# Optimization experiments

Measured on AMD Instinct MI355X. Metric: run time of the kernel, lower is better.

Reference implementation:

```python
import jax, jax.numpy as jnp
import numpy as np

B, S, E = 2, 2048, 1024
HID = 1024
HEADS = 16
EPS = 1e-5
SCALE = (E * 2) ** (-0.5)  # source uses input_data_dim*2


def setup_inputs() -> dict:
    key = jax.random.key(0)
    k1, k2, k3 = jax.random.split(key, 3)
    return {
        "x": jax.random.normal(k1, (B, S, E), dtype=jnp.float32),
        "ln_g": jnp.ones((E,), jnp.float32),
        "ln_b": jnp.zeros((E,), jnp.float32),
        "W1": jax.random.normal(k2, (E, 3 * HID), jnp.float32) * 0.02,
        "b1": jnp.zeros((3 * HID,), jnp.float32),
        "W2": jax.random.normal(k3, (HID, HID), jnp.float32) * 0.02,
        "b2": jnp.zeros((HID,), jnp.float32),
    }


def reference(x, ln_g, ln_b, W1, b1, W2, b2):
    # LayerNorm over last dim
    mu = jnp.mean(x, axis=-1, keepdims=True)
    var = jnp.mean(jnp.square(x - mu), axis=-1, keepdims=True)
    xn = (x - mu) * jax.lax.rsqrt(var + EPS) * ln_g + ln_b
    # QKV projection: [B,S,3*HID]
    qkv = jnp.einsum('bse,ef->bsf', xn, W1) + b1
    # Faithful to source: flat reshape to (heads, B, S, 3*HID/heads)
    qkv_heads = qkv.reshape(HEADS, B, S, -1)
    q, k, v = jnp.split(qkv_heads, 3, axis=-1)  # each [H,B,S,d]
    scores = jnp.einsum('hbse,hbSe->hbsS', q, k) * SCALE  # [H,B,S,S]
    att = jax.nn.softmax(scores, axis=-1)
    full_att = jnp.einsum('hbsS,hbSe->hbse', att, v)  # [H,B,S,d]
    full_att = full_att.reshape(B, S, -1)  # faithful flat reshape -> [B,S,HID]
    out = jnp.einsum('bsh,hk->bsk', full_att, W2) + b2
    return out
```

## Files before the change

kernel.cpp:

```cpp
#include <hip/hip_runtime.h>

typedef unsigned short u16;
typedef __bf16 bf16x8 __attribute__((ext_vector_type(8)));
typedef float f32x4 __attribute__((ext_vector_type(4)));

static constexpr float SCALE2 = 0.022097086912079608f * 1.4426950408889634f;

__device__ __forceinline__ u16 f2b(float f) {
  union { float f; unsigned int i; } v; v.f = f;
  unsigned int r = v.i + 0x7fffu + ((v.i >> 16) & 1u);
  return (u16)(r >> 16);
}
__device__ __forceinline__ unsigned int pk2(float a, float b) {
#if __has_builtin(__builtin_amdgcn_cvt_pk_bf16_f32)
  auto v = __builtin_amdgcn_cvt_pk_bf16_f32(a, b);
  unsigned int u;
  __builtin_memcpy(&u, &v, 4);
  return u;
#else
  union { float f; unsigned int i; } x, y; x.f = a; y.f = b;
  return ((x.i + 0x8000u) >> 16) | ((y.i + 0x8000u) & 0xffff0000u);
#endif
}
__device__ __forceinline__ void async16(const u16* g, u16* l) {
  __builtin_amdgcn_global_load_lds((const __attribute__((address_space(1))) void*)g,
                                   (__attribute__((address_space(3))) void*)l,
                                   16, 0, 0);
}

__global__ __launch_bounds__(256) void pre_kernel(const float* __restrict__ x,
                                                  const float* __restrict__ lg,
                                                  const float* __restrict__ lb,
                                                  u16* __restrict__ xn,
                                                  const float* __restrict__ W1,
                                                  u16* __restrict__ W1T,
                                                  const float* __restrict__ W2,
                                                  u16* __restrict__ W2T) {
  __shared__ __align__(16) u16 smem[64 * 72];
  const int bx = blockIdx.x;
  const int t = threadIdx.x;
  if (bx < 4096) {
    float* red = (float*)smem;
    const int row = bx;
    float4 v = *(const float4*)(x + (size_t)row * 1024 + t * 4);
    float s = v.x + v.y + v.z + v.w;
    float ss = v.x * v.x + v.y * v.y + v.z * v.z + v.w * v.w;
    for (int off = 32; off >= 1; off >>= 1) {
      s += __shfl_xor(s, off, 64);
      ss += __shfl_xor(ss, off, 64);
    }
    const int w = t >> 6;
    if ((t & 63) == 0) { red[w] = s; red[4 + w] = ss; }
    __syncthreads();
    s = red[0] + red[1] + red[2] + red[3];
    ss = red[4] + red[5] + red[6] + red[7];
    const float mu = s * (1.0f / 1024.0f);
    const float var = ss * (1.0f / 1024.0f) - mu * mu;
    const float inv = rsqrtf(var + 1e-5f);
    float4 gg = *(const float4*)(lg + t * 4);
    float4 bb = *(const float4*)(lb + t * 4);
    ushort4 o;
    o.x = f2b((v.x - mu) * inv * gg.x + bb.x);
    o.y = f2b((v.y - mu) * inv * gg.y + bb.y);
    o.z = f2b((v.z - mu) * inv * gg.z + bb.z);
    o.w = f2b((v.w - mu) * inv * gg.w + bb.w);
    *(ushort4*)(xn + (size_t)row * 1024 + t * 4) = o;
    return;
  }
  const float* in;
  u16* out;
  int C, c0, r0;
  if (bx < 4096 + 768) {
    const int idx = bx - 4096;
    C = 3072; in = W1; out = W1T;
    c0 = (idx % 48) * 64; r0 = (idx / 48) * 64;
  } else {
    const int idx = bx - 4864;
    C = 1024; in = W2; out = W2T;
    c0 = (idx % 16) * 64; r0 = (idx / 16) * 64;
  }
  const int row = t >> 2, cseg = t & 3;
  for (int it = 0; it < 4; it++) {
    float4 v = *(const float4*)&in[(size_t)(r0 + row) * C + c0 + it * 16 + cseg * 4];
    ushort4 o;
    o.x = f2b(v.x); o.y = f2b(v.y); o.z = f2b(v.z); o.w = f2b(v.w);
    *(ushort4*)&smem[row * 72 + it * 16 + cseg * 4] = o;
  }
  __syncthreads();
  const int orow = t >> 2, ch = t & 3;
  u16 vals[16];
  for (int j = 0; j < 16; j++) vals[j] = smem[(ch * 16 + j) * 72 + orow];
  u16* dp = out + (size_t)(c0 + orow) * 1024 + r0 + ch * 16;
  *(uint4*)&dp[0] = *(uint4*)&vals[0];
  *(uint4*)&dp[8] = *(uint4*)&vals[8];
}

template <int MODE, int MT>
__global__ __launch_bounds__(256) void gemm_bt(const u16* __restrict__ A,
                                               const u16* __restrict__ Bt,
                                               const float* __restrict__ bias,
                                               float* __restrict__ C,
                                               int M, int N, int K,
                                               u16* __restrict__ Qc,
                                               u16* __restrict__ Kc,
                                               u16* __restrict__ Vtmp) {
  __shared__ __align__(16) u16 SMEM[8192];
  u16* As = SMEM;
  u16* Bs = SMEM + MT * 32;
  const int m0 = blockIdx.y * MT, n0 = blockIdx.x * 128;
  const int t = threadIdx.x, w = t >> 6, lane = t & 63;
  const int q = lane >> 4, l16 = lane & 15;
  const int wm = (w >> 1) * (MT / 2), wn = (w & 1) * 64;
  constexpr int NI = MT / 32;

  const int sc = (lane & 3) ^ ((lane >> 3) & 3);
  const u16* ap = A + (size_t)(m0 + w * 16 + (lane >> 2)) * K + sc * 8;
  const u16* bp = Bt + (size_t)(n0 + w * 16 + (lane >> 2)) * K + sc * 8;
  u16* lA = &As[w * 512];
  u16* lB = &Bs[w * 512];
  const int ac = q ^ ((l16 >> 1) & 3);

  f32x4 acc[NI][4];
  const f32x4 zero = {0.f, 0.f, 0.f, 0.f};
  for (int i = 0; i < NI; i++)
    for (int j = 0; j < 4; j++) acc[i][j] = zero;

  for (int k0 = 0; k0 < K; k0 += 32) {
    for (int i = 0; i < MT / 64; i++)
      async16(ap + (size_t)(i * 64) * K, lA + i * 2048);
    for (int i = 0; i < 2; i++)
      async16(bp + (size_t)(i * 64) * K, lB + i * 2048);
    ap += 32; bp += 32;
    __syncthreads();
    bf16x8 af[NI], bfr[4];
    for (int i = 0; i < NI; i++)
      af[i] = *(const bf16x8*)&As[(wm + i * 16 + l16) * 32 + ac * 8];
    for (int j = 0; j < 4; j++)
      bfr[j] = *(const bf16x8*)&Bs[(wn + j * 16 + l16) * 32 + ac * 8];
    for (int i = 0; i < NI; i++)
      for (int j = 0; j < 4; j++)
        acc[i][j] = __builtin_amdgcn_mfma_f32_16x16x32_bf16(af[i], bfr[j], acc[i][j], 0, 0, 0);
    __syncthreads();
  }

  if constexpr (MODE == 0) {
    for (int j = 0; j < 4; j++) {
      const int col = n0 + wn + j * 16 + l16;
      const float bv = bias[col];
      for (int i = 0; i < NI; i++) {
        const int rbase = m0 + wm + i * 16 + q * 4;
        for (int r = 0; r < 4; r++)
          C[(size_t)(rbase + r) * N + col] = acc[i][j][r] + bv;
      }
    }
  } else {
    const int seg = n0 + wn;
    const int k64 = seg >> 6;
    const int tcol = k64 / 3;
    const int typ = k64 - tcol * 3;
    u16* dst = (typ == 0) ? Qc : (typ == 1) ? Kc : Vtmp;
    const float qs = (typ == 0) ? SCALE2 : 1.0f;
    const int gidx = m0 >> 7;
    u16* tw = &SMEM[w * 1280];
    float bv[4];
    for (int j = 0; j < 4; j++) bv[j] = bias[seg + j * 16 + l16];
    __syncthreads();
    for (int i = 0; i < 4; i++) {
      for (int j = 0; j < 4; j++) {
        ushort4 pk;
        pk.x = f2b((acc[i][j][0] + bv[j]) * qs);
        pk.y = f2b((acc[i][j][1] + bv[j]) * qs);
        pk.z = f2b((acc[i][j][2] + bv[j]) * qs);
        pk.w = f2b((acc[i][j][3] + bv[j]) * qs);
        *(ushort4*)&tw[(j * 16 + l16) * 20 + q * 4] = pk;
      }
      const int r2 = lane >> 2;
      const int quarter = lane & 3;
      u16 vals[16];
      for (int c = 0; c < 16; c++)
        vals[c] = tw[(quarter * 16 + c) * 20 + r2];
      const int lr = wm + i * 16 + r2;
      const int s = (lr << 4) + tcol;
      u16* dp = dst + ((size_t)gidx * 2048 + s) * 64 + quarter * 16;
      *(uint4*)&dp[0] = *(uint4*)&vals[0];
      *(uint4*)&dp[8] = *(uint4*)&vals[8];
    }
  }
}

__global__ __launch_bounds__(256) void vtrans(const u16* __restrict__ Vtmp,
                                              u16* __restrict__ Vt) {
  __shared__ __align__(16) u16 tile[64 * 64];
  const int g = blockIdx.y, s0 = blockIdx.x * 64;
  const int t = threadIdx.x;
  const int row = t >> 3, ch = t & 7;
  for (int p = 0; p < 2; p++) {
    const int r = p * 32 + row;
    uint4 v = *(const uint4*)&Vtmp[((size_t)g * 2048 + s0 + r) * 64 + ch * 8];
    *(uint4*)&tile[r * 64 + ((ch ^ (r & 7)) * 8)] = v;
  }
  __syncthreads();
  const int d = t >> 2, scn = t & 3;
  u16 vals[16];
  for (int j2 = 0; j2 < 16; j2++) {
    const int s = scn * 16 + j2;
    vals[j2] = tile[s * 64 + (((d >> 3) ^ (s & 7)) * 8) + (d & 7)];
  }
  u16* dp = Vt + ((size_t)g * 64 + d) * 2048 + s0 + scn * 16;
  *(uint4*)&dp[0] = *(uint4*)&vals[0];
  *(uint4*)&dp[8] = *(uint4*)&vals[8];
}

__global__ __launch_bounds__(256) void attn_kernel(const u16* __restrict__ Qc,
                                                   const u16* __restrict__ Kc,
                                                   const u16* __restrict__ Vt,
                                                   u16* __restrict__ Oc) {
  __shared__ __align__(16) u16 LDS[25600];
  u16* K0 = LDS;
  u16* K1 = LDS + 4096;
  u16* V0 = LDS + 8192;
  u16* V1 = LDS + 12288;
  u16* Ps = LDS + 16384;
  const int g = blockIdx.y;
  const int q0 = blockIdx.x * 128;
  const int t = threadIdx.x, w = t >> 6, lane = t & 63;
  const int q = lane >> 4, l16 = lane & 15;

  const u16* Qg = Qc + (size_t)g * 2048 * 64;
  const u16* Kg = Kc + (size_t)g * 2048 * 64;
  const u16* Vg = Vt + (size_t)g * 64 * 2048;

  bf16x8 aq[2][2];
  for (int rt = 0; rt < 2; rt++)
    for (int ks = 0; ks < 2; ks++)
      aq[rt][ks] = *(const bf16x8*)&Qg[(size_t)(q0 + w * 32 + rt * 16 + l16) * 64 + ks * 32 + q * 8];

  f32x4 accO[2][4];
  const f32x4 zero = {0.f, 0.f, 0.f, 0.f};
  for (int rt = 0; rt < 2; rt++)
    for (int c = 0; c < 4; c++) accO[rt][c] = zero;
  f32x4 psv[2] = {zero, zero};

  const int ch = (lane & 7) ^ ((lane >> 3) & 7);
  const u16* kp = Kg + (size_t)(w * 8 + (lane >> 3)) * 64 + ch * 8;
  const u16* vp = Vg + (size_t)(w * 8 + (lane >> 3)) * 2048 + ch * 8;
  u16* lK0 = K0 + w * 512;
  u16* lK1 = K1 + w * 512;
  u16* lV0 = V0 + w * 512;
  u16* lV1 = V1 + w * 512;

  const int kch = q ^ (l16 & 7);
  const int pb = w * 2304;

  for (int i = 0; i < 2; i++) {
    async16(kp + i * 2048, lK0 + i * 2048);
    async16(vp + (size_t)i * 65536, lV0 + i * 2048);
  }
  __syncthreads();

  for (int it = 0; it < 32; it++) {
    const int cur = it & 1;
    const u16* Kcur = cur ? K1 : K0;
    const u16* Vcur = cur ? V1 : V0;
    if (it < 31) {
      u16* Kn = cur ? lK0 : lK1;
      u16* Vn = cur ? lV0 : lV1;
      const int kt0 = (it + 1) * 64;
      for (int i = 0; i < 2; i++) {
        async16(kp + (size_t)kt0 * 64 + i * 2048, Kn + i * 2048);
        async16(vp + kt0 + (size_t)i * 65536, Vn + i * 2048);
      }
    }

    f32x4 sa[2][4];
    __builtin_amdgcn_s_setprio(1);
    for (int ct = 0; ct < 4; ct++) {
      bf16x8 bk0 = *(const bf16x8*)&Kcur[(ct * 16 + l16) * 64 + kch * 8];
      bf16x8 bk1 = *(const bf16x8*)&Kcur[(ct * 16 + l16) * 64 + (kch ^ 4) * 8];
      for (int rt = 0; rt < 2; rt++) {
        f32x4 a = zero;
        a = __builtin_amdgcn_mfma_f32_16x16x32_bf16(bk0, aq[rt][0], a, 0, 0, 0);
        a = __builtin_amdgcn_mfma_f32_16x16x32_bf16(bk1, aq[rt][1], a, 0, 0, 0);
        sa[rt][ct] = a;
      }
    }
    __builtin_amdgcn_s_setprio(0);

    for (int rt = 0; rt < 2; rt++) {
      u16* Pr = &Ps[pb + rt * 1152 + l16 * 72];
      for (int ct = 0; ct < 4; ct++) {
        f32x4 p;
        for (int r = 0; r < 4; r++) p[r] = __builtin_amdgcn_exp2f(sa[rt][ct][r]);
        psv[rt] += p;
        uint2 pk;
        pk.x = pk2(p[0], p[1]);
        pk.y = pk2(p[2], p[3]);
        *(uint2*)&Pr[ct * 16 + q * 4] = pk;
      }
    }

    __builtin_amdgcn_s_setprio(1);
    for (int k2 = 0; k2 < 2; k2++) {
      bf16x8 apf[2];
      for (int rt = 0; rt < 2; rt++)
        apf[rt] = *(const bf16x8*)&Ps[pb + rt * 1152 + l16 * 72 + k2 * 32 + q * 8];
      for (int c = 0; c < 4; c++) {
        const int vch = (k2 * 4 + q) ^ (l16 & 7);
        bf16x8 bv = *(const bf16x8*)&Vcur[(c * 16 + l16) * 64 + vch * 8];
        for (int rt = 0; rt < 2; rt++)
          accO[rt][c] = __builtin_amdgcn_mfma_f32_16x16x32_bf16(bv, apf[rt], accO[rt][c], 0, 0, 0);
      }
    }
    __builtin_amdgcn_s_setprio(0);

    __syncthreads();
  }

  for (int rt = 0; rt < 2; rt++) {
    float lsum = psv[rt][0] + psv[rt][1] + psv[rt][2] + psv[rt][3];
    lsum += __shfl_xor(lsum, 16, 64);
    lsum += __shfl_xor(lsum, 32, 64);
    const int srow = q0 + w * 32 + rt * 16 + l16;
    const int orow = g * 128 + (srow >> 4);
    const int cbase = (srow & 15) * 64;
    const float linv = 1.0f / lsum;
    for (int c = 0; c < 4; c++) {
      ushort4 o;
      o.x = f2b(accO[rt][c][0] * linv);
      o.y = f2b(accO[rt][c][1] * linv);
      o.z = f2b(accO[rt][c][2] * linv);
      o.w = f2b(accO[rt][c][3] * linv);
      *(ushort4*)&Oc[(size_t)orow * 1024 + cbase + c * 16 + q * 4] = o;
    }
  }
}

extern "C" void kernel_launch(void* const* d_in, const int* in_sizes, int n_in,
                              void* d_out, int out_size, void* d_ws, size_t ws_size,
                              hipStream_t stream) {
  (void)in_sizes; (void)n_in; (void)out_size; (void)ws_size;
  const float* x    = (const float*)d_in[0];
  const float* ln_g = (const float*)d_in[1];
  const float* ln_b = (const float*)d_in[2];
  const float* W1   = (const float*)d_in[3];
  const float* b1   = (const float*)d_in[4];
  const float* W2   = (const float*)d_in[5];
  const float* b2   = (const float*)d_in[6];

  char* ws = (char*)d_ws;
  u16* xn   = (u16*)(ws);
  u16* W1T  = (u16*)(ws + ((size_t)8 << 20));
  u16* W2T  = (u16*)(ws + ((size_t)14 << 20));
  u16* Qc   = (u16*)(ws + ((size_t)16 << 20));
  u16* Kc   = (u16*)(ws + ((size_t)24 << 20));
  u16* Vtmp = (u16*)(ws + ((size_t)32 << 20));
  u16* Vt   = (u16*)(ws + ((size_t)40 << 20));
  u16* Oc   = xn;

  pre_kernel<<<dim3(5120), dim3(256), 0, stream>>>(x, ln_g, ln_b, xn, W1, W1T, W2, W2T);
  gemm_bt<1, 128><<<dim3(24, 32), dim3(256), 0, stream>>>(xn, W1T, b1, nullptr,
                                                          4096, 3072, 1024, Qc, Kc, Vtmp);
  vtrans<<<dim3(32, 32), dim3(256), 0, stream>>>(Vtmp, Vt);
  attn_kernel<<<dim3(16, 32), dim3(256), 0, stream>>>(Qc, Kc, Vt, Oc);
  gemm_bt<0, 64><<<dim3(8, 64), dim3(256), 0, stream>>>(Oc, W2T, b2, (float*)d_out,
                                                        4096, 1024, 1024, nullptr, nullptr, nullptr);
}
```

Baseline: 205.9 us.

## Split attention block across 8 waves with 16 query rows each

The attention kernel now launches 512 threads per block instead of 256, so each wave owns 16 query rows rather than 32. Each thread issues one async K/V load per tile instead of two, and per-wave register state (Q fragments, accumulators, score tiles) is halved. The aim is more waves in flight to hide LDS and MFMA latency and to spread cooperative tile loads over more threads. In exchange, each K/V fragment read from LDS feeds fewer MFMAs, and more waves contend at every per-tile barrier.

```diff
diff --git a/kernel.cpp b/kernel.cpp
--- a/kernel.cpp
+++ b/kernel.cpp
@@ -211,7 +211,7 @@
   *(uint4*)&dp[8] = *(uint4*)&vals[8];
 }
 
-__global__ __launch_bounds__(256) void attn_kernel(const u16* __restrict__ Qc,
+__global__ __launch_bounds__(512) void attn_kernel(const u16* __restrict__ Qc,
                                                    const u16* __restrict__ Kc,
                                                    const u16* __restrict__ Vt,
                                                    u16* __restrict__ Oc) {
@@ -230,16 +230,14 @@
   const u16* Kg = Kc + (size_t)g * 2048 * 64;
   const u16* Vg = Vt + (size_t)g * 64 * 2048;
 
-  bf16x8 aq[2][2];
-  for (int rt = 0; rt < 2; rt++)
-    for (int ks = 0; ks < 2; ks++)
-      aq[rt][ks] = *(const bf16x8*)&Qg[(size_t)(q0 + w * 32 + rt * 16 + l16) * 64 + ks * 32 + q * 8];
-
-  f32x4 accO[2][4];
+  bf16x8 aq[2];
+  for (int ks = 0; ks < 2; ks++)
+    aq[ks] = *(const bf16x8*)&Qg[(size_t)(q0 + w * 16 + l16) * 64 + ks * 32 + q * 8];
+
+  f32x4 accO[4];
   const f32x4 zero = {0.f, 0.f, 0.f, 0.f};
-  for (int rt = 0; rt < 2; rt++)
-    for (int c = 0; c < 4; c++) accO[rt][c] = zero;
-  f32x4 psv[2] = {zero, zero};
+  for (int c = 0; c < 4; c++) accO[c] = zero;
+  f32x4 psv = zero;
 
   const int ch = (lane & 7) ^ ((lane >> 3) & 7);
   const u16* kp = Kg + (size_t)(w * 8 + (lane >> 3)) * 64 + ch * 8;
@@ -250,12 +248,10 @@
   u16* lV1 = V1 + w * 512;
 
   const int kch = q ^ (l16 & 7);
-  const int pb = w * 2304;
-
-  for (int i = 0; i < 2; i++) {
-    async16(kp + i * 2048, lK0 + i * 2048);
-    async16(vp + (size_t)i * 65536, lV0 + i * 2048);
-  }
+  const int pb = w * 1152;
+
+  async16(kp, lK0);
+  async16(vp, lV0);
   __syncthreads();
 
   for (int it = 0; it < 32; it++) {
@@ -263,35 +259,29 @@
     const u16* Kcur = cur ? K1 : K0;
     const u16* Vcur = cur ? V1 : V0;
     if (it < 31) {
-      u16* Kn = cur ? lK0 : lK1;
-      u16* Vn = cur ? lV0 : lV1;
       const int kt0 = (it + 1) * 64;
-      for (int i = 0; i < 2; i++) {
-        async16(kp + (size_t)kt0 * 64 + i * 2048, Kn + i * 2048);
-        async16(vp + kt0 + (size_t)i * 65536, Vn + i * 2048);
-      }
-    }
-
-    f32x4 sa[2][4];
+      async16(kp + (size_t)kt0 * 64, cur ? lK0 : lK1);
+      async16(vp + kt0, cur ? lV0 : lV1);
+    }
+
+    f32x4 sa[4];
     __builtin_amdgcn_s_setprio(1);
     for (int ct = 0; ct < 4; ct++) {
       bf16x8 bk0 = *(const bf16x8*)&Kcur[(ct * 16 + l16) * 64 + kch * 8];
       bf16x8 bk1 = *(const bf16x8*)&Kcur[(ct * 16 + l16) * 64 + (kch ^ 4) * 8];
-      for (int rt = 0; rt < 2; rt++) {
-        f32x4 a = zero;
-        a = __builtin_amdgcn_mfma_f32_16x16x32_bf16(bk0, aq[rt][0], a, 0, 0, 0);
-        a = __builtin_amdgcn_mfma_f32_16x16x32_bf16(bk1, aq[rt][1], a, 0, 0, 0);
-        sa[rt][ct] = a;
-      }
+      f32x4 a = zero;
+      a = __builtin_amdgcn_mfma_f32_16x16x32_bf16(bk0, aq[0], a, 0, 0, 0);
+      a = __builtin_amdgcn_mfma_f32_16x16x32_bf16(bk1, aq[1], a, 0, 0, 0);
+      sa[ct] = a;
     }
     __builtin_amdgcn_s_setprio(0);
 
-    for (int rt = 0; rt < 2; rt++) {
-      u16* Pr = &Ps[pb + rt * 1152 + l16 * 72];
+    {
+      u16* Pr = &Ps[pb + l16 * 72];
       for (int ct = 0; ct < 4; ct++) {
         f32x4 p;
-        for (int r = 0; r < 4; r++) p[r] = __builtin_amdgcn_exp2f(sa[rt][ct][r]);
-        psv[rt] += p;
+        for (int r = 0; r < 4; r++) p[r] = __builtin_amdgcn_exp2f(sa[ct][r]);
+        psv += p;
         uint2 pk;
         pk.x = pk2(p[0], p[1]);
         pk.y = pk2(p[2], p[3]);
@@ -301,14 +291,11 @@
 
     __builtin_amdgcn_s_setprio(1);
     for (int k2 = 0; k2 < 2; k2++) {
-      bf16x8 apf[2];
-      for (int rt = 0; rt < 2; rt++)
-        apf[rt] = *(const bf16x8*)&Ps[pb + rt * 1152 + l16 * 72 + k2 * 32 + q * 8];
+      bf16x8 apf = *(const bf16x8*)&Ps[pb + l16 * 72 + k2 * 32 + q * 8];
       for (int c = 0; c < 4; c++) {
         const int vch = (k2 * 4 + q) ^ (l16 & 7);
         bf16x8 bv = *(const bf16x8*)&Vcur[(c * 16 + l16) * 64 + vch * 8];
-        for (int rt = 0; rt < 2; rt++)
-          accO[rt][c] = __builtin_amdgcn_mfma_f32_16x16x32_bf16(bv, apf[rt], accO[rt][c], 0, 0, 0);
+        accO[c] = __builtin_amdgcn_mfma_f32_16x16x32_bf16(bv, apf, accO[c], 0, 0, 0);
       }
     }
     __builtin_amdgcn_s_setprio(0);
@@ -316,20 +303,20 @@
     __syncthreads();
   }
 
-  for (int rt = 0; rt < 2; rt++) {
-    float lsum = psv[rt][0] + psv[rt][1] + psv[rt][2] + psv[rt][3];
+  {
+    float lsum = psv[0] + psv[1] + psv[2] + psv[3];
     lsum += __shfl_xor(lsum, 16, 64);
     lsum += __shfl_xor(lsum, 32, 64);
-    const int srow = q0 + w * 32 + rt * 16 + l16;
+    const int srow = q0 + w * 16 + l16;
     const int orow = g * 128 + (srow >> 4);
     const int cbase = (srow & 15) * 64;
     const float linv = 1.0f / lsum;
     for (int c = 0; c < 4; c++) {
       ushort4 o;
-      o.x = f2b(accO[rt][c][0] * linv);
-      o.y = f2b(accO[rt][c][1] * linv);
-      o.z = f2b(accO[rt][c][2] * linv);
-      o.w = f2b(accO[rt][c][3] * linv);
+      o.x = f2b(accO[c][0] * linv);
+      o.y = f2b(accO[c][1] * linv);
+      o.z = f2b(accO[c][2] * linv);
+      o.w = f2b(accO[c][3] * linv);
       *(ushort4*)&Oc[(size_t)orow * 1024 + cbase + c * 16 + q * 4] = o;
     }
   }
@@ -361,7 +348,7 @@
   gemm_bt<1, 128><<<dim3(24, 32), dim3(256), 0, stream>>>(xn, W1T, b1, nullptr,
                                                           4096, 3072, 1024, Qc, Kc, Vtmp);
   vtrans<<<dim3(32, 32), dim3(256), 0, stream>>>(Vtmp, Vt);
-  attn_kernel<<<dim3(16, 32), dim3(256), 0, stream>>>(Qc, Kc, Vt, Oc);
+  attn_kernel<<<dim3(16, 32), dim3(512), 0, stream>>>(Qc, Kc, Vt, Oc);
   gemm_bt<0, 64><<<dim3(8, 64), dim3(256), 0, stream>>>(Oc, W2T, b2, (float*)d_out,
                                                         4096, 1024, 1024, nullptr, nullptr, nullptr);
 }
```

After: 196.3 us. -4.7%, faster.
